# Optimization experiments

Measured on AMD Instinct MI355X. Metric: run time of the kernel, lower is better.

## Reference

```python
import jax, jax.numpy as jnp
import numpy as np

EPS_GEN = 1e-7   # GENConv message epsilon
LN_EPS = 1e-5    # torch LayerNorm default eps


def _ln(x, g, b):
    mu = x.mean(-1, keepdims=True)
    v = ((x - mu) ** 2).mean(-1, keepdims=True)
    return (x - mu) / jnp.sqrt(v + LN_EPS) * g + b


def _genconv(x, src, dst, N, t, W1, b1, g1, be1, W2, b2):
    # GENConv(aggr='softmax', learn_t, num_layers=2, norm='layer'), no edge_attr
    msg = jax.nn.relu(x[src]) + EPS_GEN                 # [E,H] gather + eps
    z = msg * t
    m = jax.ops.segment_max(z, dst, num_segments=N)      # scatter-max [N,H]
    e = jnp.exp(z - m[dst])
    denom = jax.ops.segment_sum(e, dst, num_segments=N) + 1e-16
    alpha = e / denom[dst]                               # per-neighborhood softmax
    out = jax.ops.segment_sum(msg * alpha, dst, num_segments=N) + x  # aggregate + root
    h = jax.nn.relu(_ln(out @ W1 + b1, g1, be1))         # MLP [H,2H] + LN + ReLU
    return h @ W2 + b2                                   # [2H,H] plain last layer


def setup_inputs():
    key = jax.random.key(0)
    ks = jax.random.split(key, 24)
    N, E, Fin, H = 100000, 1600000, 16, 64
    s = 0.02
    d = {
        'x': jax.random.normal(ks[0], (N, Fin), jnp.float32),
        'edge_index': jax.random.randint(ks[1], (2, E), 0, N, dtype=jnp.int32),
        'W_enc': jax.random.normal(ks[2], (Fin, H), jnp.float32) * s,
        'b_enc': jnp.zeros((H,), jnp.float32),
        't1': jnp.float32(1.0),
        'W1a': jax.random.normal(ks[3], (H, 2 * H), jnp.float32) * s,
        'b1a': jnp.zeros((2 * H,), jnp.float32),
        'g1a': jnp.ones((2 * H,), jnp.float32),
        'be1a': jnp.zeros((2 * H,), jnp.float32),
        'W1b': jax.random.normal(ks[4], (2 * H, H), jnp.float32) * s,
        'b1b': jnp.zeros((H,), jnp.float32),
        'g_n1': jnp.ones((H,), jnp.float32),
        'b_n1': jnp.zeros((H,), jnp.float32),
        't2': jnp.float32(1.0),
        'W2a': jax.random.normal(ks[5], (H, 2 * H), jnp.float32) * s,
        'b2a': jnp.zeros((2 * H,), jnp.float32),
        'g2a': jnp.ones((2 * H,), jnp.float32),
        'be2a': jnp.zeros((2 * H,), jnp.float32),
        'W2b': jax.random.normal(ks[6], (2 * H, H), jnp.float32) * s,
        'b2b': jnp.zeros((H,), jnp.float32),
        'g_n0': jnp.ones((H,), jnp.float32),
        'b_n0': jnp.zeros((H,), jnp.float32),
        'W_lin': jax.random.normal(ks[7], (H, 1), jnp.float32) * s,
        'b_lin': jnp.zeros((1,), jnp.float32),
    }
    return d


def reference(x, edge_index, W_enc, b_enc, t1, W1a, b1a, g1a, be1a, W1b, b1b,
              g_n1, b_n1, t2, W2a, b2a, g2a, be2a, W2b, b2b, g_n0, b_n0,
              W_lin, b_lin):
    N = x.shape[0]
    src, dst = edge_index[0], edge_index[1]
    h = x @ W_enc + b_enc                                   # node encoder
    h = _genconv(h, src, dst, N, t1, W1a, b1a, g1a, be1a, W1b, b1b)  # layers[0].conv (bare)
    # layers[1]: DeepGCNLayer res+ -> x + conv(act(norm(x)))  (dropout = identity, deterministic ref)
    r = _genconv(jax.nn.relu(_ln(h, g_n1, b_n1)), src, dst, N, t2,
                 W2a, b2a, g2a, be2a, W2b, b2b)
    h = h + r
    h = jax.nn.relu(_ln(h, g_n0, b_n0))                     # layers[0].norm / act at the end
    logits = h @ W_lin + b_lin                              # [N,1]
    return jax.nn.sigmoid(logits), logits
```

## Files before the change

### kernel.cpp

```cpp
#include <hip/hip_runtime.h>
#include <math.h>

constexpr int HD   = 64;
constexpr int HD2  = 128;
constexpr int SCAP = 48;
constexpr int NPW  = 4;
constexpr int NPB  = 16;
constexpr int PSH  = 14;
constexpr int EPB  = 2048;

constexpr float FXS  = 8192.f;
constexpr float FXSI = 1.f / 8192.f;

__device__ __forceinline__ unsigned short fix16(float v) {
    int q = (int)(fmaxf(v, 0.f) * FXS + 0.5f);
    return (unsigned short)min(q, 65535);
}

__device__ __forceinline__ float wave_sum(float v) {
#pragma unroll
    for (int off = 32; off > 0; off >>= 1) v += __shfl_xor(v, off, 64);
    return v;
}

__global__ void prep_kernel(const int* __restrict__ ei,
                            int* __restrict__ cursor, int* __restrict__ slots,
                            const float* __restrict__ x,
                            const float* __restrict__ W,
                            const float* __restrict__ b,
                            float* __restrict__ h,
                            unsigned short* __restrict__ g,
                            int E, int N, int SB) {
    if (blockIdx.x < (unsigned)SB) {
        int p = blockIdx.x & 7;
        int base = (blockIdx.x >> 3) * EPB;
        for (int off = threadIdx.x; off < EPB; off += 256) {
            int e = base + off;
            if (e < E) {
                int dst = ei[E + e];
                if ((dst >> PSH) == p) {
                    int src = ei[e];
                    int pos = atomicAdd(&cursor[dst], 1);
                    if (pos < SCAP) slots[(size_t)dst * SCAP + pos] = src;
                }
            }
        }
    } else {
        int i = (blockIdx.x - SB) * 256 + threadIdx.x;
        if (i >= N * HD) return;
        int n = i >> 6, j = i & 63;
        const float* xr = x + (size_t)n * 16;
        float acc = b[j];
#pragma unroll
        for (int k = 0; k < 16; k++) acc += xr[k] * W[k * HD + j];
        h[i] = acc;
        g[i] = fix16(acc);
    }
}

template <int MODE>
__global__ void __launch_bounds__(256, 6) conv_kernel(
    const unsigned short* __restrict__ gin,
    const float* __restrict__ hroot,
    const int* __restrict__ deg_arr, const int* __restrict__ slots,
    const float* __restrict__ tptr,
    const float* __restrict__ W1, const float* __restrict__ b1,
    const float* __restrict__ g1, const float* __restrict__ be1,
    const float* __restrict__ W2, const float* __restrict__ b2,
    const float* __restrict__ gn, const float* __restrict__ bn,
    const float* __restrict__ resid,
    const float* __restrict__ wlin, const float* __restrict__ blin,
    float* __restrict__ outA, unsigned short* __restrict__ outG, int N) {
    __shared__ float s_out[NPB][HD];
    __shared__ float s_h[NPB][HD2];
    int wv = threadIdx.x >> 6, j = threadIdx.x & 63;
    int q = j >> 4;
    int c = (j & 15) << 2;
    int nb = blockIdx.x * NPB + wv * NPW;
    float t = tptr[0];

    int deg[NPW], sid[NPW];
#pragma unroll
    for (int u = 0; u < NPW; u++) {
        int n = nb + u;
        int d = (n < N) ? min(deg_arr[n], SCAP) : 0;
        deg[u] = d;
        sid[u] = (j < d) ? slots[(size_t)n * SCAP + j] : 0;
    }

#pragma unroll
    for (int u = 0; u < NPW; u++) {
        int n = nb + u;
        if (n < N) {
            int d = deg[u];
            float4 ae = {0.f, 0.f, 0.f, 0.f}, aw = {0.f, 0.f, 0.f, 0.f};
            for (int base = 0; base < d; base += 16) {
#pragma unroll
                for (int bb = 0; bb < 4; bb++) {
                    int i = base + bb * 4 + q;
                    int s = __shfl(sid[u], i, 64);
                    if (i < d) {
                        ushort4 uv = *(const ushort4*)(gin + (size_t)s * HD + c);
                        float m0 = fmaf((float)uv.x, FXSI, 1e-7f);
                        float m1 = fmaf((float)uv.y, FXSI, 1e-7f);
                        float m2 = fmaf((float)uv.z, FXSI, 1e-7f);
                        float m3 = fmaf((float)uv.w, FXSI, 1e-7f);
                        float e0 = __expf(m0 * t), e1 = __expf(m1 * t);
                        float e2 = __expf(m2 * t), e3 = __expf(m3 * t);
                        ae.x += e0; ae.y += e1; ae.z += e2; ae.w += e3;
                        aw.x = fmaf(m0, e0, aw.x); aw.y = fmaf(m1, e1, aw.y);
                        aw.z = fmaf(m2, e2, aw.z); aw.w = fmaf(m3, e3, aw.w);
                    }
                }
            }
#pragma unroll
            for (int off = 16; off <= 32; off <<= 1) {
                ae.x += __shfl_xor(ae.x, off, 64); ae.y += __shfl_xor(ae.y, off, 64);
                ae.z += __shfl_xor(ae.z, off, 64); ae.w += __shfl_xor(ae.w, off, 64);
                aw.x += __shfl_xor(aw.x, off, 64); aw.y += __shfl_xor(aw.y, off, 64);
                aw.z += __shfl_xor(aw.z, off, 64); aw.w += __shfl_xor(aw.w, off, 64);
            }
            if (q == 0) {
                float4 o;
                if (MODE == 0) {
                    float4 hv = *(const float4*)(hroot + (size_t)n * HD + c);
                    o.x = aw.x / (ae.x + 1e-16f) + hv.x;
                    o.y = aw.y / (ae.y + 1e-16f) + hv.y;
                    o.z = aw.z / (ae.z + 1e-16f) + hv.z;
                    o.w = aw.w / (ae.w + 1e-16f) + hv.w;
                } else {
                    ushort4 uv = *(const ushort4*)(gin + (size_t)n * HD + c);
                    o.x = aw.x / (ae.x + 1e-16f) + (float)uv.x * FXSI;
                    o.y = aw.y / (ae.y + 1e-16f) + (float)uv.y * FXSI;
                    o.z = aw.z / (ae.z + 1e-16f) + (float)uv.z * FXSI;
                    o.w = aw.w / (ae.w + 1e-16f) + (float)uv.w * FXSI;
                }
                *(float4*)&s_out[wv * NPW + u][c] = o;
            }
        }
    }

    float acc0[NPW], acc1[NPW];
    {
        float b1a_ = b1[j], b1b_ = b1[HD + j];
#pragma unroll
        for (int u = 0; u < NPW; u++) { acc0[u] = b1a_; acc1[u] = b1b_; }
    }
#pragma unroll 2
    for (int kk = 0; kk < HD; kk += 4) {
        float w0[4], w1[4];
#pragma unroll
        for (int r = 0; r < 4; r++) {
            w0[r] = W1[(kk + r) * HD2 + j];
            w1[r] = W1[(kk + r) * HD2 + HD + j];
        }
#pragma unroll
        for (int u = 0; u < NPW; u++) {
            float4 sv = *(const float4*)&s_out[wv * NPW + u][kk];
            acc0[u] = fmaf(sv.x, w0[0], acc0[u]); acc0[u] = fmaf(sv.y, w0[1], acc0[u]);
            acc0[u] = fmaf(sv.z, w0[2], acc0[u]); acc0[u] = fmaf(sv.w, w0[3], acc0[u]);
            acc1[u] = fmaf(sv.x, w1[0], acc1[u]); acc1[u] = fmaf(sv.y, w1[1], acc1[u]);
            acc1[u] = fmaf(sv.z, w1[2], acc1[u]); acc1[u] = fmaf(sv.w, w1[3], acc1[u]);
        }
    }
    {
        float g1a_ = g1[j], g1b_ = g1[HD + j];
        float be1a_ = be1[j], be1b_ = be1[HD + j];
#pragma unroll
        for (int u = 0; u < NPW; u++) {
            float mu = wave_sum(acc0[u] + acc1[u]) * (1.f / HD2);
            float d0 = acc0[u] - mu, d1 = acc1[u] - mu;
            float var = wave_sum(d0 * d0 + d1 * d1) * (1.f / HD2);
            float rstd = rsqrtf(var + 1e-5f);
            s_h[wv * NPW + u][j]      = fmaxf(d0 * rstd * g1a_ + be1a_, 0.f);
            s_h[wv * NPW + u][HD + j] = fmaxf(d1 * rstd * g1b_ + be1b_, 0.f);
        }
    }

    float y[NPW];
    {
        float b2_ = b2[j];
#pragma unroll
        for (int u = 0; u < NPW; u++) y[u] = b2_;
    }
#pragma unroll 2
    for (int kk = 0; kk < HD2; kk += 4) {
        float w[4];
#pragma unroll
        for (int r = 0; r < 4; r++) w[r] = W2[(kk + r) * HD + j];
#pragma unroll
        for (int u = 0; u < NPW; u++) {
            float4 sv = *(const float4*)&s_h[wv * NPW + u][kk];
            y[u] = fmaf(sv.x, w[0], y[u]); y[u] = fmaf(sv.y, w[1], y[u]);
            y[u] = fmaf(sv.z, w[2], y[u]); y[u] = fmaf(sv.w, w[3], y[u]);
        }
    }

    float gn_ = gn[j], bn_ = bn[j];
    float wl = (MODE == 1) ? wlin[j] : 0.f;
#pragma unroll
    for (int u = 0; u < NPW; u++) {
        int n = nb + u;
        if (n >= N) continue;
        if (MODE == 0) {
            float yv = y[u];
            outA[(size_t)n * HD + j] = yv;
            float mu = wave_sum(yv) * (1.f / HD);
            float d = yv - mu;
            float var = wave_sum(d * d) * (1.f / HD);
            float rstd = rsqrtf(var + 1e-5f);
            outG[(size_t)n * HD + j] = fix16(d * rstd * gn_ + bn_);
        } else {
            float hf = y[u] + resid[(size_t)n * HD + j];
            float mu = wave_sum(hf) * (1.f / HD);
            float d = hf - mu;
            float var = wave_sum(d * d) * (1.f / HD);
            float rstd = rsqrtf(var + 1e-5f);
            float h2 = fmaxf(d * rstd * gn_ + bn_, 0.f);
            float dot = wave_sum(h2 * wl);
            if (j == 0) {
                float logit = dot + blin[0];
                outA[n] = 1.f / (1.f + __expf(-logit));
                outA[N + n] = logit;
            }
        }
    }
}

extern "C" void kernel_launch(void* const* d_in, const int* in_sizes, int n_in,
                              void* d_out, int out_size, void* d_ws, size_t ws_size,
                              hipStream_t stream) {
    const float* x     = (const float*)d_in[0];
    const int*   ei    = (const int*)  d_in[1];
    const float* W_enc = (const float*)d_in[2];
    const float* b_enc = (const float*)d_in[3];
    const float* t1    = (const float*)d_in[4];
    const float* W1a   = (const float*)d_in[5];
    const float* b1a   = (const float*)d_in[6];
    const float* g1a   = (const float*)d_in[7];
    const float* be1a  = (const float*)d_in[8];
    const float* W1b   = (const float*)d_in[9];
    const float* b1b   = (const float*)d_in[10];
    const float* g_n1  = (const float*)d_in[11];
    const float* b_n1  = (const float*)d_in[12];
    const float* t2    = (const float*)d_in[13];
    const float* W2a   = (const float*)d_in[14];
    const float* b2a   = (const float*)d_in[15];
    const float* g2a   = (const float*)d_in[16];
    const float* be2a  = (const float*)d_in[17];
    const float* W2b   = (const float*)d_in[18];
    const float* b2b   = (const float*)d_in[19];
    const float* g_n0  = (const float*)d_in[20];
    const float* b_n0  = (const float*)d_in[21];
    const float* W_lin = (const float*)d_in[22];
    const float* b_lin = (const float*)d_in[23];

    int N = in_sizes[0] / 16;
    int E = in_sizes[1] / 2;
    size_t NH = (size_t)N * HD;

    float* h0           = (float*)d_ws;
    float* h1           = h0 + NH;
    unsigned short* g0  = (unsigned short*)(h1 + NH);
    unsigned short* g1f = g0 + NH;
    int*   cursor       = (int*)(g1f + NH);
    int*   slots        = cursor + N;

    int nodeBlocks = (N + NPB - 1) / NPB;
    int chunks     = (E + EPB - 1) / EPB;
    int SB         = chunks * 8;
    int encBlocks  = (int)((NH + 255) / 256);

    hipMemsetAsync(cursor, 0, (size_t)N * sizeof(int), stream);

    prep_kernel<<<SB + encBlocks, 256, 0, stream>>>(ei, cursor, slots,
                                                    x, W_enc, b_enc, h0, g0,
                                                    E, N, SB);

    conv_kernel<0><<<nodeBlocks, 256, 0, stream>>>(g0, h0, cursor, slots, t1,
                                                   W1a, b1a, g1a, be1a, W1b, b1b,
                                                   g_n1, b_n1, nullptr, nullptr, nullptr,
                                                   h1, g1f, N);

    conv_kernel<1><<<nodeBlocks, 256, 0, stream>>>(g1f, nullptr, cursor, slots, t2,
                                                   W2a, b2a, g2a, be2a, W2b, b2b,
                                                   g_n0, b_n0, h1, W_lin, b_lin,
                                                   (float*)d_out, nullptr, N);
}
```

Measured before the change: 443.3 us.

## Run node MLP matmuls on MFMA with split-bf16 three-pass emulation

The two per-node dense layers (64->128, 128->64) now run on bf16 MFMA 16x16x32 instructions instead of scalar FMA loops. FP32 accuracy is kept by splitting activations and weights into hi and lo bf16 parts and issuing three MFMAs per tile. The weights are pre-split and pre-swizzled into MFMA fragment layout by extra blocks in the prep kernel, plus a second small prep launch. Intermediates now pass through shared memory with several extra __syncthreads, and the occupancy hint in launch bounds was dropped, so the saving in matmul ALU work is traded against more LDS traffic, synchronisation and one added launch.

```diff
diff --git a/kernel.cpp b/kernel.cpp
--- a/kernel.cpp
+++ b/kernel.cpp
@@ -9,8 +9,15 @@
 constexpr int PSH  = 14;
 constexpr int EPB  = 2048;
 
+constexpr int SO = 68;
+constexpr int SU = 132;
+constexpr int SY = 68;
+
 constexpr float FXS  = 8192.f;
 constexpr float FXSI = 1.f / 8192.f;
+
+typedef short  bf16x8 __attribute__((ext_vector_type(8)));
+typedef float  f32x4  __attribute__((ext_vector_type(4)));
 
 __device__ __forceinline__ unsigned short fix16(float v) {
     int q = (int)(fmaxf(v, 0.f) * FXS + 0.5f);
@@ -21,6 +28,21 @@
 #pragma unroll
     for (int off = 32; off > 0; off >>= 1) v += __shfl_xor(v, off, 64);
     return v;
+}
+
+__device__ __forceinline__ void splitf(float f, short& hi, short& lo) {
+    unsigned u = __float_as_uint(f);
+    hi = (short)(u >> 16);
+    float lf = f - __uint_as_float(u & 0xffff0000u);
+    lo = (short)(__float_as_uint(lf) >> 16);
+}
+
+__device__ __forceinline__ void split8(const float* p, bf16x8& hi, bf16x8& lo) {
+    float v[8];
+    *(float4*)&v[0] = *(const float4*)p;
+    *(float4*)&v[4] = *(const float4*)(p + 4);
+#pragma unroll
+    for (int j = 0; j < 8; j++) { short h, l; splitf(v[j], h, l); hi[j] = h; lo[j] = l; }
 }
 
 __global__ void prep_kernel(const int* __restrict__ ei,
@@ -30,7 +52,10 @@
                             const float* __restrict__ b,
                             float* __restrict__ h,
                             unsigned short* __restrict__ g,
-                            int E, int N, int SB) {
+                            const float* __restrict__ W1, const float* __restrict__ W2,
+                            short* __restrict__ W1hi, short* __restrict__ W1lo,
+                            short* __restrict__ W2hi, short* __restrict__ W2lo,
+                            int E, int N, int SB, int encB) {
     if (blockIdx.x < (unsigned)SB) {
         int p = blockIdx.x & 7;
         int base = (blockIdx.x >> 3) * EPB;
@@ -45,7 +70,7 @@
                 }
             }
         }
-    } else {
+    } else if (blockIdx.x < (unsigned)(SB + encB)) {
         int i = (blockIdx.x - SB) * 256 + threadIdx.x;
         if (i >= N * HD) return;
         int n = i >> 6, j = i & 63;
@@ -55,24 +80,51 @@
         for (int k = 0; k < 16; k++) acc += xr[k] * W[k * HD + j];
         h[i] = acc;
         g[i] = fix16(acc);
+    } else {
+        int idx = (blockIdx.x - SB - encB) * 256 + threadIdx.x;
+        if (idx < 1024) {
+            int ks = idx >> 9, rem = idx & 511;
+            int nt = rem >> 6, lane = rem & 63;
+#pragma unroll
+            for (int j = 0; j < 8; j++) {
+                int k = ks * 32 + (lane >> 4) * 8 + j;
+                int n = nt * 16 + (lane & 15);
+                short hh, ll; splitf(W1[k * HD2 + n], hh, ll);
+                W1hi[idx * 8 + j] = hh; W1lo[idx * 8 + j] = ll;
+            }
+        } else if (idx < 2048) {
+            int jdx = idx - 1024;
+            int ks = jdx >> 8, rem = jdx & 255;
+            int nt = rem >> 6, lane = rem & 63;
+#pragma unroll
+            for (int j = 0; j < 8; j++) {
+                int k = ks * 32 + (lane >> 4) * 8 + j;
+                int n = nt * 16 + (lane & 15);
+                short hh, ll; splitf(W2[k * HD + n], hh, ll);
+                W2hi[jdx * 8 + j] = hh; W2lo[jdx * 8 + j] = ll;
+            }
+        }
     }
 }
 
 template <int MODE>
-__global__ void __launch_bounds__(256, 6) conv_kernel(
+__global__ void __launch_bounds__(256) conv_kernel(
     const unsigned short* __restrict__ gin,
     const float* __restrict__ hroot,
     const int* __restrict__ deg_arr, const int* __restrict__ slots,
     const float* __restrict__ tptr,
-    const float* __restrict__ W1, const float* __restrict__ b1,
+    const short* __restrict__ W1hi, const short* __restrict__ W1lo,
+    const float* __restrict__ b1,
     const float* __restrict__ g1, const float* __restrict__ be1,
-    const float* __restrict__ W2, const float* __restrict__ b2,
+    const short* __restrict__ W2hi, const short* __restrict__ W2lo,
+    const float* __restrict__ b2,
     const float* __restrict__ gn, const float* __restrict__ bn,
     const float* __restrict__ resid,
     const float* __restrict__ wlin, const float* __restrict__ blin,
     float* __restrict__ outA, unsigned short* __restrict__ outG, int N) {
-    __shared__ float s_out[NPB][HD];
-    __shared__ float s_h[NPB][HD2];
+    __shared__ float s_out[NPB][SO];
+    __shared__ float s_u[NPB][SU];
+    __shared__ float s_y[NPB][SY];
     int wv = threadIdx.x >> 6, j = threadIdx.x & 63;
     int q = j >> 4;
     int c = (j & 15) << 2;
@@ -87,10 +139,10 @@
         deg[u] = d;
         sid[u] = (j < d) ? slots[(size_t)n * SCAP + j] : 0;
     }
-
 #pragma unroll
     for (int u = 0; u < NPW; u++) {
         int n = nb + u;
+        int bl = wv * NPW + u;
         if (n < N) {
             int d = deg[u];
             float4 ae = {0.f, 0.f, 0.f, 0.f}, aw = {0.f, 0.f, 0.f, 0.f};
@@ -135,66 +187,82 @@
                     o.z = aw.z / (ae.z + 1e-16f) + (float)uv.z * FXSI;
                     o.w = aw.w / (ae.w + 1e-16f) + (float)uv.w * FXSI;
                 }
-                *(float4*)&s_out[wv * NPW + u][c] = o;
-            }
-        }
-    }
-
-    float acc0[NPW], acc1[NPW];
+                *(float4*)&s_out[bl][c] = o;
+            }
+        } else if (q == 0) {
+            float4 z = {0.f, 0.f, 0.f, 0.f};
+            *(float4*)&s_out[bl][c] = z;
+        }
+    }
+    __syncthreads();
+
+    int mrow = j & 15, kq = j >> 4, ncol = j & 15;
     {
-        float b1a_ = b1[j], b1b_ = b1[HD + j];
-#pragma unroll
-        for (int u = 0; u < NPW; u++) { acc0[u] = b1a_; acc1[u] = b1b_; }
-    }
-#pragma unroll 2
-    for (int kk = 0; kk < HD; kk += 4) {
-        float w0[4], w1[4];
-#pragma unroll
-        for (int r = 0; r < 4; r++) {
-            w0[r] = W1[(kk + r) * HD2 + j];
-            w1[r] = W1[(kk + r) * HD2 + HD + j];
-        }
-#pragma unroll
-        for (int u = 0; u < NPW; u++) {
-            float4 sv = *(const float4*)&s_out[wv * NPW + u][kk];
-            acc0[u] = fmaf(sv.x, w0[0], acc0[u]); acc0[u] = fmaf(sv.y, w0[1], acc0[u]);
-            acc0[u] = fmaf(sv.z, w0[2], acc0[u]); acc0[u] = fmaf(sv.w, w0[3], acc0[u]);
-            acc1[u] = fmaf(sv.x, w1[0], acc1[u]); acc1[u] = fmaf(sv.y, w1[1], acc1[u]);
-            acc1[u] = fmaf(sv.z, w1[2], acc1[u]); acc1[u] = fmaf(sv.w, w1[3], acc1[u]);
-        }
-    }
+        f32x4 acc[2];
+#pragma unroll
+        for (int i = 0; i < 2; i++) {
+            float bb = b1[(wv * 2 + i) * 16 + ncol];
+            acc[i] = (f32x4){bb, bb, bb, bb};
+        }
+#pragma unroll
+        for (int ks = 0; ks < 2; ks++) {
+            bf16x8 ah, al;
+            split8(&s_out[mrow][ks * 32 + kq * 8], ah, al);
+#pragma unroll
+            for (int i = 0; i < 2; i++) {
+                int nt = wv * 2 + i;
+                int fo = (((ks * 8 + nt) * 64 + j) << 3);
+                bf16x8 bh = *(const bf16x8*)(W1hi + fo);
+                bf16x8 bl = *(const bf16x8*)(W1lo + fo);
+                acc[i] = __builtin_amdgcn_mfma_f32_16x16x32_bf16(al, bh, acc[i], 0, 0, 0);
+                acc[i] = __builtin_amdgcn_mfma_f32_16x16x32_bf16(ah, bl, acc[i], 0, 0, 0);
+                acc[i] = __builtin_amdgcn_mfma_f32_16x16x32_bf16(ah, bh, acc[i], 0, 0, 0);
+            }
+        }
+#pragma unroll
+        for (int i = 0; i < 2; i++)
+#pragma unroll
+            for (int r = 0; r < 4; r++)
+                s_u[kq * 4 + r][(wv * 2 + i) * 16 + ncol] = acc[i][r];
+    }
+    __syncthreads();
+
     {
         float g1a_ = g1[j], g1b_ = g1[HD + j];
         float be1a_ = be1[j], be1b_ = be1[HD + j];
 #pragma unroll
         for (int u = 0; u < NPW; u++) {
-            float mu = wave_sum(acc0[u] + acc1[u]) * (1.f / HD2);
-            float d0 = acc0[u] - mu, d1 = acc1[u] - mu;
+            int bl = wv * NPW + u;
+            float u0 = s_u[bl][j], u1 = s_u[bl][HD + j];
+            float mu = wave_sum(u0 + u1) * (1.f / HD2);
+            float d0 = u0 - mu, d1 = u1 - mu;
             float var = wave_sum(d0 * d0 + d1 * d1) * (1.f / HD2);
             float rstd = rsqrtf(var + 1e-5f);
-            s_h[wv * NPW + u][j]      = fmaxf(d0 * rstd * g1a_ + be1a_, 0.f);
-            s_h[wv * NPW + u][HD + j] = fmaxf(d1 * rstd * g1b_ + be1b_, 0.f);
-        }
-    }
-
-    float y[NPW];
+            s_u[bl][j]      = fmaxf(d0 * rstd * g1a_ + be1a_, 0.f);
+            s_u[bl][HD + j] = fmaxf(d1 * rstd * g1b_ + be1b_, 0.f);
+        }
+    }
+    __syncthreads();
+
     {
-        float b2_ = b2[j];
-#pragma unroll
-        for (int u = 0; u < NPW; u++) y[u] = b2_;
-    }
-#pragma unroll 2
-    for (int kk = 0; kk < HD2; kk += 4) {
-        float w[4];
-#pragma unroll
-        for (int r = 0; r < 4; r++) w[r] = W2[(kk + r) * HD + j];
-#pragma unroll
-        for (int u = 0; u < NPW; u++) {
-            float4 sv = *(const float4*)&s_h[wv * NPW + u][kk];
-            y[u] = fmaf(sv.x, w[0], y[u]); y[u] = fmaf(sv.y, w[1], y[u]);
-            y[u] = fmaf(sv.z, w[2], y[u]); y[u] = fmaf(sv.w, w[3], y[u]);
-        }
-    }
+        float bb = b2[wv * 16 + ncol];
+        f32x4 acc = (f32x4){bb, bb, bb, bb};
+#pragma unroll
+        for (int ks = 0; ks < 4; ks++) {
+            bf16x8 ah, al;
+            split8(&s_u[mrow][ks * 32 + kq * 8], ah, al);
+            int fo = (((ks * 4 + wv) * 64 + j) << 3);
+            bf16x8 bh = *(const bf16x8*)(W2hi + fo);
+            bf16x8 bl = *(const bf16x8*)(W2lo + fo);
+            acc = __builtin_amdgcn_mfma_f32_16x16x32_bf16(al, bh, acc, 0, 0, 0);
+            acc = __builtin_amdgcn_mfma_f32_16x16x32_bf16(ah, bl, acc, 0, 0, 0);
+            acc = __builtin_amdgcn_mfma_f32_16x16x32_bf16(ah, bh, acc, 0, 0, 0);
+        }
+#pragma unroll
+        for (int r = 0; r < 4; r++)
+            s_y[kq * 4 + r][wv * 16 + ncol] = acc[r];
+    }
+    __syncthreads();
 
     float gn_ = gn[j], bn_ = bn[j];
     float wl = (MODE == 1) ? wlin[j] : 0.f;
@@ -202,8 +270,8 @@
     for (int u = 0; u < NPW; u++) {
         int n = nb + u;
         if (n >= N) continue;
+        float yv = s_y[wv * NPW + u][j];
         if (MODE == 0) {
-            float yv = y[u];
             outA[(size_t)n * HD + j] = yv;
             float mu = wave_sum(yv) * (1.f / HD);
             float d = yv - mu;
@@ -211,7 +279,7 @@
             float rstd = rsqrtf(var + 1e-5f);
             outG[(size_t)n * HD + j] = fix16(d * rstd * gn_ + bn_);
         } else {
-            float hf = y[u] + resid[(size_t)n * HD + j];
+            float hf = yv + resid[(size_t)n * HD + j];
             float mu = wave_sum(hf) * (1.f / HD);
             float d = hf - mu;
             float var = wave_sum(d * d) * (1.f / HD);
@@ -265,6 +333,14 @@
     unsigned short* g1f = g0 + NH;
     int*   cursor       = (int*)(g1f + NH);
     int*   slots        = cursor + N;
+    short* W1hi_1       = (short*)(slots + (size_t)N * SCAP);
+    short* W1lo_1       = W1hi_1 + 8192;
+    short* W2hi_1       = W1lo_1 + 8192;
+    short* W2lo_1       = W2hi_1 + 8192;
+    short* W1hi_2       = W2lo_1 + 8192;
+    short* W1lo_2       = W1hi_2 + 8192;
+    short* W2hi_2       = W1lo_2 + 8192;
+    short* W2lo_2       = W2hi_2 + 8192;
 
     int nodeBlocks = (N + NPB - 1) / NPB;
     int chunks     = (E + EPB - 1) / EPB;
@@ -273,17 +349,21 @@
 
     hipMemsetAsync(cursor, 0, (size_t)N * sizeof(int), stream);
 
-    prep_kernel<<<SB + encBlocks, 256, 0, stream>>>(ei, cursor, slots,
-                                                    x, W_enc, b_enc, h0, g0,
-                                                    E, N, SB);
-
-    conv_kernel<0><<<nodeBlocks, 256, 0, stream>>>(g0, h0, cursor, slots, t1,
-                                                   W1a, b1a, g1a, be1a, W1b, b1b,
-                                                   g_n1, b_n1, nullptr, nullptr, nullptr,
-                                                   h1, g1f, N);
-
-    conv_kernel<1><<<nodeBlocks, 256, 0, stream>>>(g1f, nullptr, cursor, slots, t2,
-                                                   W2a, b2a, g2a, be2a, W2b, b2b,
-                                                   g_n0, b_n0, h1, W_lin, b_lin,
-                                                   (float*)d_out, nullptr, N);
-}
+    prep_kernel<<<SB + encBlocks + 8, 256, 0, stream>>>(
+        ei, cursor, slots, x, W_enc, b_enc, h0, g0,
+        W1a, W1b, W1hi_1, W1lo_1, W2hi_1, W2lo_1, E, N, SB, encBlocks);
+
+    prep_kernel<<<8, 256, 0, stream>>>(
+        ei, cursor, slots, x, W_enc, b_enc, h0, g0,
+        W2a, W2b, W1hi_2, W1lo_2, W2hi_2, W2lo_2, E, N, 0, 0);
+
+    conv_kernel<0><<<nodeBlocks, 256, 0, stream>>>(
+        g0, h0, cursor, slots, t1,
+        W1hi_1, W1lo_1, b1a, g1a, be1a, W2hi_1, W2lo_1, b1b,
+        g_n1, b_n1, nullptr, nullptr, nullptr, h1, g1f, N);
+
+    conv_kernel<1><<<nodeBlocks, 256, 0, stream>>>(
+        g1f, nullptr, cursor, slots, t2,
+        W1hi_2, W1lo_2, b2a, g2a, be2a, W2hi_2, W2lo_2, b2b,
+        g_n0, b_n0, h1, W_lin, b_lin, (float*)d_out, nullptr, N);
+}
```

New measurement: 412.4 us. 1.07x faster.
